# Performance work log

Measured on AMD Instinct MI355X. Metric: run time of the kernel, lower is better.

Reference implementation:

```python
import jax, jax.numpy as jnp
import numpy as np

N = 2_000_000
H, W = 50, 50
BIRTH_RANGE = (0.0, 1.0)
PERS_RANGE = (0.0, 1.0)
EPS = 1e-08


def setup_inputs() -> dict:
    key = jax.random.key(0)
    k1, = jax.random.split(key, 1)
    # (birth, death) pairs in [0,1); math is identical regardless of death>=birth
    pairs = jax.random.uniform(k1, (N, 2), dtype=jnp.float32)
    sigma = jnp.float32(0.1)  # learnable scalar parameter
    grid_x = jnp.linspace(BIRTH_RANGE[0], BIRTH_RANGE[1], W, dtype=jnp.float32)
    grid_y = jnp.linspace(PERS_RANGE[0], PERS_RANGE[1], H, dtype=jnp.float32)
    return {"pairs": pairs, "sigma": sigma, "grid_x": grid_x, "grid_y": grid_y}


def reference(pairs, sigma, grid_x, grid_y):
    birth = pairs[:, 0]
    pers = pairs[:, 1] - pairs[:, 0]
    # normalize into grid coordinates (default ranges are (0,1))
    birth_norm = (birth - BIRTH_RANGE[0]) / (BIRTH_RANGE[1] - BIRTH_RANGE[0] + EPS)
    pers_norm = (pers - PERS_RANGE[0]) / (PERS_RANGE[1] - PERS_RANGE[0] + EPS)
    weights = pers  # weight_fn == 'linear'
    inv2s2 = 1.0 / (2.0 * sigma * sigma)
    # separable Gaussian splat: [N, W] and [N, H]
    gx = jnp.exp(-((grid_x[None, :] - birth_norm[:, None]) ** 2) * inv2s2)
    gy = jnp.exp(-((grid_y[None, :] - pers_norm[:, None]) ** 2) * inv2s2)
    # sum_i w_i * outer(gy_i, gx_i), without materializing [N, H, W]
    image = jnp.einsum('n,nh,nw->hw', weights, gy, gx)
    return image / (image.max() + EPS)
```

## Files before the change

### kernel.cpp

```cpp
#include <hip/hip_runtime.h>

#define HH 50
#define WW 50
#define EPSF 1e-8f

#define BXH 128
#define BYH 96
#define Y0F (-0.5f)
#define YSPAN 1.5f
#define REPSZ (BXH * BYH)

#define GXOFF 0
#define GYOFF (GXOFF + WW * BXH)
#define POFF  (GYOFF + HH * BYH)
#define IMGOFF (POFF + BYH * WW)
#define CNTOFF (IMGOFF + HH * WW + 12)
#define REPOFF (CNTOFF + 4)

__device__ __forceinline__ unsigned bf16pk(float a, float b) {
    unsigned ua = __float_as_uint(a), ub = __float_as_uint(b);
    ua = (ua + 0x7FFFu + ((ua >> 16) & 1u)) >> 16;
    ub = (ub + 0x7FFFu + ((ub >> 16) & 1u)) >> 16;
    return ua | (ub << 16);
}

__device__ __forceinline__ void splat1(float b, float death, float* hist) {
    const float p = death - b;
    if (p < Y0F) return;
    int ix = (int)(b * (float)BXH);
    int iy = (int)((p - Y0F) * 64.0f);
    ix = min(ix, BXH - 1);
    iy = min(iy, BYH - 1);
    atomicAdd(&hist[iy * BXH + ix], p);
}

__global__ __launch_bounds__(1024) void pie_hist_lds(
    const float4* __restrict__ pairs4, int n,
    const float* __restrict__ grid_x, const float* __restrict__ grid_y,
    const float* __restrict__ sigma_p, float* __restrict__ ws, int R)
{
    __shared__ float hist[REPSZ];
    const int t = threadIdx.x;

    {
        const float4 z = make_float4(0.f, 0.f, 0.f, 0.f);
        float4* h4 = (float4*)hist;
        #pragma unroll
        for (int i = t; i < REPSZ / 4; i += 1024) h4[i] = z;
    }

    if (blockIdx.x == 0) {
        if (t == 0) ((int*)ws)[CNTOFF] = 0;
        const float s = *sigma_p;
        const float a = 1.0f / (2.0f * s * s);
        for (int i = t; i < WW * BXH; i += 1024) {
            const int w = i >> 7, ix = i & (BXH - 1);
            const float c = (ix + 0.5f) * (1.0f / BXH);
            const float d = grid_x[w] - c;
            ws[GXOFF + i] = __expf(-d * d * a);
        }
        for (int i = t; i < HH * BYH; i += 1024) {
            const int h = i / BYH, iy = i - h * BYH;
            const float c = Y0F + (iy + 0.5f) * (YSPAN / (float)BYH);
            const float d = grid_y[h] - c;
            ws[GYOFF + i] = __expf(-d * d * a);
        }
    }
    __syncthreads();

    const int n2 = n >> 1;
    const int stride = R * 1024;
    #pragma unroll 4
    for (int i = blockIdx.x * 1024 + t; i < n2; i += stride) {
        const float4 q = pairs4[i];
        splat1(q.x, q.y, hist);
        splat1(q.z, q.w, hist);
    }
    if ((n & 1) && blockIdx.x == 0 && t == 0) {
        const float2 last = ((const float2*)pairs4)[n - 1];
        splat1(last.x, last.y, hist);
    }
    __syncthreads();

    uint4* dst = (uint4*)((char*)ws + (size_t)REPOFF * 4 + (size_t)blockIdx.x * (REPSZ * 2));
    const float4* src = (const float4*)hist;
    #pragma unroll
    for (int i = t; i < REPSZ / 8; i += 1024) {
        const float4 a = src[2 * i], b = src[2 * i + 1];
        uint4 o;
        o.x = bf16pk(a.x, a.y); o.y = bf16pk(a.z, a.w);
        o.z = bf16pk(b.x, b.y); o.w = bf16pk(b.z, b.w);
        dst[i] = o;
    }
}

__global__ __launch_bounds__(640) void pie_c1(float* __restrict__ ws, int R)
{
    __shared__ float part[40 * BXH];
    __shared__ float row[BXH];
    __shared__ float gxl[WW * (BXH + 1)];
    const int t = threadIdx.x;
    const int rowi = blockIdx.x;

    for (int i = t; i < WW * BXH; i += 640) {
        const int w = i >> 7, ix = i & (BXH - 1);
        gxl[w * (BXH + 1) + ix] = ws[GXOFF + i];
    }

    const int g = t >> 4;
    const int s = t & 15;
    {
        const char* repbase = (const char*)ws + (size_t)REPOFF * 4;
        float a0 = 0.f, a1 = 0.f, a2 = 0.f, a3 = 0.f;
        float a4 = 0.f, a5 = 0.f, a6 = 0.f, a7 = 0.f;
        #pragma unroll 4
        for (int r = g; r < R; r += 40) {
            const uint4 u = *(const uint4*)(repbase + (size_t)r * (REPSZ * 2)
                                            + (size_t)(rowi * 16 + s) * 16);
            a0 += __uint_as_float(u.x << 16);
            a1 += __uint_as_float(u.x & 0xFFFF0000u);
            a2 += __uint_as_float(u.y << 16);
            a3 += __uint_as_float(u.y & 0xFFFF0000u);
            a4 += __uint_as_float(u.z << 16);
            a5 += __uint_as_float(u.z & 0xFFFF0000u);
            a6 += __uint_as_float(u.w << 16);
            a7 += __uint_as_float(u.w & 0xFFFF0000u);
        }
        float4* p4 = (float4*)(part + g * BXH + s * 8);
        p4[0] = make_float4(a0, a1, a2, a3);
        p4[1] = make_float4(a4, a5, a6, a7);
    }
    __syncthreads();

    if (t < BXH) {
        float sum = 0.0f;
        #pragma unroll
        for (int k = 0; k < 40; ++k) sum += part[k * BXH + t];
        row[t] = sum;
    }
    __syncthreads();

    if (t < WW) {
        float acc = 0.0f;
        #pragma unroll 4
        for (int k = 0; k < BXH; ++k)
            acc += row[k] * gxl[t * (BXH + 1) + k];
        ws[POFF + rowi * WW + t] = acc;
    }
}

__global__ __launch_bounds__(256) void pie_c2(float* __restrict__ ws,
                                              float* __restrict__ out)
{
    __shared__ float part[4 * WW];
    __shared__ float redmax[4];
    __shared__ int is_last;
    const int h = blockIdx.x;
    const int t = threadIdx.x;

    if (t < 4 * WW) {
        const int w = t % WW;
        const int c = t / WW;
        const float* gy = ws + GYOFF + h * BYH;
        const float* P  = ws + POFF;
        const int r0 = c * (BYH / 4);
        float acc = 0.0f;
        #pragma unroll 4
        for (int r = r0; r < r0 + BYH / 4; ++r)
            acc += gy[r] * P[r * WW + w];
        part[t] = acc;
    }
    __syncthreads();
    if (t < WW)
        ws[IMGOFF + h * WW + t] = part[t] + part[WW + t] + part[2 * WW + t]
                                + part[3 * WW + t];
    __threadfence();
    __syncthreads();
    if (t == 0) {
        const int old = atomicAdd((int*)ws + CNTOFF, 1);
        is_last = (old == HH - 1);
    }
    __syncthreads();
    if (!is_last) return;
    __threadfence();

    float m = -1e30f;
    for (int i = t; i < HH * WW; i += 256) m = fmaxf(m, ws[IMGOFF + i]);
    #pragma unroll
    for (int off = 32; off > 0; off >>= 1)
        m = fmaxf(m, __shfl_down(m, off));
    const int wv = t >> 6, ln = t & 63;
    if (ln == 0) redmax[wv] = m;
    __syncthreads();
    if (t == 0)
        redmax[0] = fmaxf(fmaxf(redmax[0], redmax[1]), fmaxf(redmax[2], redmax[3]));
    __syncthreads();

    const float inv = 1.0f / (redmax[0] + EPSF);
    for (int i = t; i < HH * WW; i += 256) out[i] = ws[IMGOFF + i] * inv;
}

extern "C" void kernel_launch(void* const* d_in, const int* in_sizes, int n_in,
                              void* d_out, int out_size, void* d_ws, size_t ws_size,
                              hipStream_t stream) {
    const float4* pairs4 = (const float4*)d_in[0];
    const float*  sigma  = (const float*)d_in[1];
    const float*  grid_x = (const float*)d_in[2];
    const float*  grid_y = (const float*)d_in[3];
    float* ws  = (float*)d_ws;
    float* out = (float*)d_out;
    const int n = in_sizes[0] / 2;

    const long avail_bytes = (long)ws_size - (long)REPOFF * 4;
    long cap = avail_bytes / (REPSZ * 2);
    int R = (int)(cap < 256 ? cap : 256);
    if (R < 1) R = 1;

    pie_hist_lds<<<R, 1024, 0, stream>>>(pairs4, n, grid_x, grid_y, sigma, ws, R);
    pie_c1<<<BYH, 640, 0, stream>>>(ws, R);
    pie_c2<<<HH, 256, 0, stream>>>(ws, out);
}
```

Before: 96.94 us.

## Fuse final reduction kernel into row-reduce kernel via last-block pattern

```diff
diff --git a/kernel.cpp b/kernel.cpp
--- a/kernel.cpp
+++ b/kernel.cpp
@@ -94,15 +94,21 @@
     }
 }
 
-__global__ __launch_bounds__(640) void pie_c1(float* __restrict__ ws, int R)
+__global__ __launch_bounds__(1024) void pie_c1(float* __restrict__ ws,
+                                               float* __restrict__ out, int R)
 {
-    __shared__ float part[40 * BXH];
+    __shared__ float part[64 * BXH];
     __shared__ float row[BXH];
     __shared__ float gxl[WW * (BXH + 1)];
+    __shared__ float Pl[BYH * WW];
+    __shared__ float gyl[HH * BYH];
+    __shared__ float imgl[HH * WW];
+    __shared__ float redmax[16];
+    __shared__ int is_last;
     const int t = threadIdx.x;
     const int rowi = blockIdx.x;
 
-    for (int i = t; i < WW * BXH; i += 640) {
+    for (int i = t; i < WW * BXH; i += 1024) {
         const int w = i >> 7, ix = i & (BXH - 1);
         gxl[w * (BXH + 1) + ix] = ws[GXOFF + i];
     }
@@ -114,7 +120,7 @@
         float a0 = 0.f, a1 = 0.f, a2 = 0.f, a3 = 0.f;
         float a4 = 0.f, a5 = 0.f, a6 = 0.f, a7 = 0.f;
         #pragma unroll 4
-        for (int r = g; r < R; r += 40) {
+        for (int r = g; r < R; r += 64) {
             const uint4 u = *(const uint4*)(repbase + (size_t)r * (REPSZ * 2)
                                             + (size_t)(rowi * 16 + s) * 16);
             a0 += __uint_as_float(u.x << 16);
@@ -135,7 +141,7 @@
     if (t < BXH) {
         float sum = 0.0f;
         #pragma unroll
-        for (int k = 0; k < 40; ++k) sum += part[k * BXH + t];
+        for (int k = 0; k < 64; ++k) sum += part[k * BXH + t];
         row[t] = sum;
     }
     __syncthreads();
@@ -147,57 +153,59 @@
             acc += row[k] * gxl[t * (BXH + 1) + k];
         ws[POFF + rowi * WW + t] = acc;
     }
-}
-
-__global__ __launch_bounds__(256) void pie_c2(float* __restrict__ ws,
-                                              float* __restrict__ out)
-{
-    __shared__ float part[4 * WW];
-    __shared__ float redmax[4];
-    __shared__ int is_last;
-    const int h = blockIdx.x;
-    const int t = threadIdx.x;
-
-    if (t < 4 * WW) {
-        const int w = t % WW;
-        const int c = t / WW;
-        const float* gy = ws + GYOFF + h * BYH;
-        const float* P  = ws + POFF;
-        const int r0 = c * (BYH / 4);
-        float acc = 0.0f;
-        #pragma unroll 4
-        for (int r = r0; r < r0 + BYH / 4; ++r)
-            acc += gy[r] * P[r * WW + w];
-        part[t] = acc;
-    }
-    __syncthreads();
-    if (t < WW)
-        ws[IMGOFF + h * WW + t] = part[t] + part[WW + t] + part[2 * WW + t]
-                                + part[3 * WW + t];
     __threadfence();
     __syncthreads();
     if (t == 0) {
         const int old = atomicAdd((int*)ws + CNTOFF, 1);
-        is_last = (old == HH - 1);
+        is_last = (old == BYH - 1);
     }
     __syncthreads();
     if (!is_last) return;
     __threadfence();
 
+    for (int i = t; i < BYH * WW; i += 1024) Pl[i]  = ws[POFF + i];
+    for (int i = t; i < HH * BYH; i += 1024) gyl[i] = ws[GYOFF + i];
+    __syncthreads();
+
+    if (t < 800) {
+        const int w = t >> 4, rc = t & 15;
+        const int r0 = rc * 6;
+        const float p0 = Pl[(r0 + 0) * WW + w];
+        const float p1 = Pl[(r0 + 1) * WW + w];
+        const float p2 = Pl[(r0 + 2) * WW + w];
+        const float p3 = Pl[(r0 + 3) * WW + w];
+        const float p4 = Pl[(r0 + 4) * WW + w];
+        const float p5 = Pl[(r0 + 5) * WW + w];
+        for (int h = 0; h < HH; ++h) {
+            const float* gyr = gyl + h * BYH + r0;
+            float acc = gyr[0] * p0 + gyr[1] * p1 + gyr[2] * p2
+                      + gyr[3] * p3 + gyr[4] * p4 + gyr[5] * p5;
+            acc += __shfl_xor(acc, 1, 16);
+            acc += __shfl_xor(acc, 2, 16);
+            acc += __shfl_xor(acc, 4, 16);
+            acc += __shfl_xor(acc, 8, 16);
+            if (rc == 0) imgl[h * WW + w] = acc;
+        }
+    }
+    __syncthreads();
+
     float m = -1e30f;
-    for (int i = t; i < HH * WW; i += 256) m = fmaxf(m, ws[IMGOFF + i]);
+    for (int i = t; i < HH * WW; i += 1024) m = fmaxf(m, imgl[i]);
     #pragma unroll
     for (int off = 32; off > 0; off >>= 1)
         m = fmaxf(m, __shfl_down(m, off));
-    const int wv = t >> 6, ln = t & 63;
-    if (ln == 0) redmax[wv] = m;
-    __syncthreads();
-    if (t == 0)
-        redmax[0] = fmaxf(fmaxf(redmax[0], redmax[1]), fmaxf(redmax[2], redmax[3]));
+    if ((t & 63) == 0) redmax[t >> 6] = m;
+    __syncthreads();
+    if (t == 0) {
+        float mm = redmax[0];
+        #pragma unroll
+        for (int k = 1; k < 16; ++k) mm = fmaxf(mm, redmax[k]);
+        redmax[0] = mm;
+    }
     __syncthreads();
 
     const float inv = 1.0f / (redmax[0] + EPSF);
-    for (int i = t; i < HH * WW; i += 256) out[i] = ws[IMGOFF + i] * inv;
+    for (int i = t; i < HH * WW; i += 1024) out[i] = imgl[i] * inv;
 }
 
 extern "C" void kernel_launch(void* const* d_in, const int* in_sizes, int n_in,
@@ -217,6 +225,5 @@
     if (R < 1) R = 1;
 
     pie_hist_lds<<<R, 1024, 0, stream>>>(pairs4, n, grid_x, grid_y, sigma, ws, R);
-    pie_c1<<<BYH, 640, 0, stream>>>(ws, R);
-    pie_c2<<<HH, 256, 0, stream>>>(ws, out);
-}
+    pie_c1<<<BYH, 1024, 0, stream>>>(ws, out, R);
+}
```

Measured after the change: 123.7 us. 1.28x slower.
